# Performance work log

Measured on AMD Instinct MI355X. Metric: run time of the kernel, lower is better.

Reference implementation:

```python
import jax, jax.numpy as jnp
import numpy as np

D_HEAD = 64
MASK_FILL = -1000000.0


def setup_inputs() -> dict:
    key = jax.random.key(0)
    ks = jax.random.split(key, 5)
    batch, seq, d_model, n_heads, d_head = 4, 2048, 1024, 16, D_HEAD
    # xavier_uniform bound for [d_model, n_heads, d_head]: treated as fan_in=d_model, fan_out=n_heads*d_head
    bound_qkv = float(np.sqrt(6.0 / (d_model + n_heads * d_head)))
    bound_out = float(np.sqrt(6.0 / (d_head + n_heads * d_model)))
    return {
        "resid": jax.random.normal(ks[0], (batch, seq, d_model), dtype=jnp.float32),
        "W_Q": jax.random.uniform(ks[1], (d_model, n_heads, d_head), jnp.float32, -bound_qkv, bound_qkv),
        "W_K": jax.random.uniform(ks[2], (d_model, n_heads, d_head), jnp.float32, -bound_qkv, bound_qkv),
        "W_V": jax.random.uniform(ks[3], (d_model, n_heads, d_head), jnp.float32, -bound_qkv, bound_qkv),
        "W_out": jax.random.uniform(ks[4], (d_head, n_heads, d_model), jnp.float32, -bound_out, bound_out),
        "b_out": jnp.zeros((d_model,), dtype=jnp.float32),
    }


def reference(resid, W_Q, W_K, W_V, W_out, b_out):
    # resid: [b, s, d]; W_Q/K/V: [d, h, dh]; W_out: [dh, h, d]
    seq = resid.shape[1]
    d_head = W_Q.shape[-1]
    q = jnp.einsum('bsd,dhk->bshk', resid, W_Q)
    k = jnp.einsum('bsd,dhk->bshk', resid, W_K)
    v = jnp.einsum('bsd,dhk->bshk', resid, W_V)
    scores = jnp.einsum('bqhk,bkhd->bhqd', q, k.astype(q.dtype)) if False else jnp.einsum('bqhc,bshc->bhqs', q, k)
    scores = scores / jnp.sqrt(jnp.asarray(d_head, dtype=scores.dtype))
    causal_mask = jnp.triu(jnp.ones((seq, seq), dtype=bool), k=1)
    scores = jnp.where(causal_mask, MASK_FILL, scores)
    probs = jax.nn.softmax(scores, axis=-1)  # [b, h, q, s]
    z = jnp.einsum('bhqs,bshc->bqhc', probs, v)
    out = jnp.einsum('bqhc,chd->bqd', z, W_out) + b_out
    return out
```

## Files before the change

### kernel.cpp

```cpp
#include <hip/hip_runtime.h>
#include <hip/hip_bf16.h>


typedef short s16x8 __attribute__((ext_vector_type(8)));
typedef short s16x4 __attribute__((ext_vector_type(4)));
typedef float f32x4 __attribute__((ext_vector_type(4)));

#define MFMA_BF16(A, B, C) __builtin_amdgcn_mfma_f32_16x16x32_bf16((A), (B), (C), 0, 0, 0)

#if __has_builtin(__builtin_amdgcn_exp2f)
#define EXP2(x) __builtin_amdgcn_exp2f(x)
#else
#define EXP2(x) exp2f(x)
#endif
#if __has_builtin(__builtin_amdgcn_rcpf)
#define RCP(x) __builtin_amdgcn_rcpf(x)
#else
#define RCP(x) (1.0f / (x))
#endif

__device__ __forceinline__ short f2bf(float f) {
    __bf16 h = (__bf16)f;
    return __builtin_bit_cast(short, h);
}

__device__ __forceinline__ void gld16(const unsigned short* g, unsigned short* l) {
    __builtin_amdgcn_global_load_lds(
        (const __attribute__((address_space(1))) unsigned int*)g,
        (__attribute__((address_space(3))) unsigned int*)l, 16, 0, 0);
}

__global__ __launch_bounds__(256) void prep_fused(
    const float* __restrict__ resid, const float* __restrict__ WQ,
    const float* __restrict__ WK, const float* __restrict__ WV,
    const float* __restrict__ Wout,
    unsigned short* __restrict__ residb, unsigned short* __restrict__ Wqkvt,
    unsigned short* __restrict__ W2t)
{
    const int bid = blockIdx.x;
    if (bid < 8192) {
        const int i = bid * 256 + threadIdx.x;
        const float4 v = ((const float4*)resid)[i];
        s16x4 o;
        o[0] = f2bf(v.x); o[1] = f2bf(v.y); o[2] = f2bf(v.z); o[3] = f2bf(v.w);
        *(s16x4*)(residb + (size_t)i * 4) = o;
        return;
    }
    __shared__ unsigned short tile[64][66];
    const int id2 = bid - 8192;
    const int which = id2 >> 8;
    const int sub = id2 & 255;
    const int tx = threadIdx.x & 63, ty = threadIdx.x >> 6;
    if (which < 3) {
        const float* W = which == 0 ? WQ : (which == 1 ? WK : WV);
        unsigned short* Wt = Wqkvt + (size_t)which * 1024 * 1024;
        const int n0 = (sub & 15) * 64, k0 = (sub >> 4) * 64;
        #pragma unroll
        for (int i = ty; i < 64; i += 4)
            tile[i][tx] = (unsigned short)f2bf(W[(size_t)(k0 + i) * 1024 + n0 + tx]);
        __syncthreads();
        #pragma unroll
        for (int i = ty; i < 64; i += 4)
            Wt[(size_t)(n0 + i) * 1024 + k0 + tx] = tile[tx][i];
    } else {
        const int d0 = (sub & 15) * 64, h = sub >> 4;
        #pragma unroll
        for (int c = ty; c < 64; c += 4)
            tile[c][tx] = (unsigned short)f2bf(Wout[(size_t)(c * 16 + h) * 1024 + d0 + tx]);
        __syncthreads();
        #pragma unroll
        for (int i = ty; i < 64; i += 4)
            W2t[(size_t)(d0 + i) * 1024 + h * 64 + tx] = tile[tx][i];
    }
}

template <int MODE>
__global__ __launch_bounds__(256, 2) void gemm_bt(
    const unsigned short* __restrict__ A,
    const unsigned short* __restrict__ Bt,
    float* __restrict__ Cf, const float* __restrict__ bias,
    unsigned short* __restrict__ Qb, unsigned short* __restrict__ Kb,
    unsigned short* __restrict__ Vt,
    int M, int N, int K)
{
    __shared__ __align__(16) unsigned short AB[2 * 128 * 72];
    const int tid  = threadIdx.x;
    const int lane = tid & 63;
    const int w    = tid >> 6;
    const int wm   = w & 1, wn = w >> 1;
    const int quad = lane >> 4, fl = lane & 15;
    const int m0 = blockIdx.y * 128, n0 = blockIdx.x * 128;

    const unsigned short* gp[9];
    unsigned ldso[9];
    #pragma unroll
    for (int i = 0; i < 9; ++i) {
        const int c = i * 256 + tid;
        const int cm = c % 1152;
        const int r = cm / 9, cl0 = cm % 9;
        const int cl = (cl0 == 8) ? 0 : cl0;
        gp[i] = (c < 1152 ? A + (size_t)(m0 + r) * K : Bt + (size_t)(n0 + r) * K) + cl * 8;
        ldso[i] = (unsigned)c * 8u;
    }

    f32x4 acc[4][4];
    #pragma unroll
    for (int i = 0; i < 4; ++i)
        #pragma unroll
        for (int j = 0; j < 4; ++j)
            acc[i][j] = (f32x4){0.f, 0.f, 0.f, 0.f};

    for (int kt = 0; kt < K; kt += 64) {
        __syncthreads();
        #pragma unroll
        for (int i = 0; i < 9; ++i)
            gld16(gp[i] + kt, AB + ldso[i]);
        __syncthreads();
        #pragma unroll
        for (int ko = 0; ko < 2; ++ko) {
            s16x8 af[4], bf[4];
            #pragma unroll
            for (int mi = 0; mi < 4; ++mi)
                af[mi] = *(const s16x8*)(AB + (wm * 64 + mi * 16 + fl) * 72 + ko * 32 + quad * 8);
            #pragma unroll
            for (int ni = 0; ni < 4; ++ni)
                bf[ni] = *(const s16x8*)(AB + 9216 + (wn * 64 + ni * 16 + fl) * 72 + ko * 32 + quad * 8);
            #pragma unroll
            for (int mi = 0; mi < 4; ++mi)
                #pragma unroll
                for (int ni = 0; ni < 4; ++ni)
                    acc[mi][ni] = MFMA_BF16(af[mi], bf[ni], acc[mi][ni]);
        }
    }

    if (MODE == 0) {
        #pragma unroll
        for (int ni = 0; ni < 4; ++ni) {
            const int col = n0 + wn * 64 + ni * 16 + fl;
            const float bv = bias[col];
            #pragma unroll
            for (int mi = 0; mi < 4; ++mi) {
                const int row = m0 + wm * 64 + mi * 16 + quad * 4;
                #pragma unroll
                for (int r = 0; r < 4; ++r)
                    Cf[(size_t)(row + r) * N + col] = acc[mi][ni][r] + bv;
            }
        }
    } else {
        #pragma unroll
        for (int ni = 0; ni < 4; ++ni) {
            const int colg = n0 + wn * 64 + ni * 16 + fl;
            #pragma unroll
            for (int mi = 0; mi < 4; ++mi) {
                const int token = m0 + wm * 64 + mi * 16 + quad * 4;
                if (n0 < 1024) {
                    #pragma unroll
                    for (int r = 0; r < 4; ++r)
                        Qb[(size_t)(token + r) * 1024 + colg] = (unsigned short)f2bf(acc[mi][ni][r]);
                } else if (n0 < 2048) {
                    #pragma unroll
                    for (int r = 0; r < 4; ++r)
                        Kb[(size_t)(token + r) * 1024 + (colg - 1024)] = (unsigned short)f2bf(acc[mi][ni][r]);
                } else {
                    const int cc = colg - 2048;
                    const int hh = cc >> 6, cl = cc & 63;
                    const int bb = token >> 11, ss = token & 2047;
                    s16x4 pv;
                    pv[0] = f2bf(acc[mi][ni][0]); pv[1] = f2bf(acc[mi][ni][1]);
                    pv[2] = f2bf(acc[mi][ni][2]); pv[3] = f2bf(acc[mi][ni][3]);
                    *(s16x4*)(Vt + (size_t)((bb * 16 + hh) * 64 + cl) * 2048 + ss) = pv;
                }
            }
        }
    }
}

template <bool DIAG>
__device__ __forceinline__ void attn_tile(
    int s0, int wl, int wq0, int fl, int quad,
    const unsigned short* __restrict__ KV, const unsigned short* __restrict__ Vs,
    unsigned short* __restrict__ PbW,
    const s16x8 (&qfr)[2][2], f32x4 (&zt)[2][4], float (&ls)[2])
{
    const float SC = 0.18033688011112042f;
    const float M  = 32.0f;
    #pragma unroll
    for (int c4 = 0; c4 < 4; ++c4) {
        if (DIAG && c4 > wl) break;
        #pragma unroll
        for (int e = 0; e < 2; ++e) {
            const int f = 2 * c4 + e;
            const unsigned short* Krow = KV + (f * 16 + fl) * 72;
            const s16x8 kf0 = *(const s16x8*)(Krow + quad * 8);
            const s16x8 kf1 = *(const s16x8*)(Krow + 32 + quad * 8);
            #pragma unroll
            for (int g = 0; g < 2; ++g) {
                unsigned short* pw = PbW + (g * 16 + fl) * 36 + e * 16 + quad * 4;
                if (DIAG && f > 2 * wl + g) {
                    *(s16x4*)pw = (s16x4){0, 0, 0, 0};
                } else {
                    f32x4 z = (f32x4){0.f, 0.f, 0.f, 0.f};
                    z = MFMA_BF16(kf0, qfr[g][0], z);
                    z = MFMA_BF16(kf1, qfr[g][1], z);
                    float p[4];
                    #pragma unroll
                    for (int r = 0; r < 4; ++r) {
                        float arg = fmaf(z[r], SC, -M);
                        if (DIAG && f == 2 * wl + g) {
                            const int s = s0 + f * 16 + quad * 4 + r;
                            const int qi = wq0 + g * 16 + fl;
                            if (s > qi) arg = -100.f;
                        }
                        p[r] = EXP2(arg);
                    }
                    ls[g] += (p[0] + p[1]) + (p[2] + p[3]);
                    s16x4 pk;
                    pk[0] = f2bf(p[0]); pk[1] = f2bf(p[1]);
                    pk[2] = f2bf(p[2]); pk[3] = f2bf(p[3]);
                    *(s16x4*)pw = pk;
                }
            }
        }
        const s16x8 pf0 = *(const s16x8*)(PbW + fl * 36 + quad * 8);
        const s16x8 pf1 = *(const s16x8*)(PbW + (16 + fl) * 36 + quad * 8);
        #pragma unroll
        for (int mf = 0; mf < 4; ++mf) {
            const s16x8 vf = *(const s16x8*)(Vs + (mf * 16 + fl) * 136 + c4 * 32 + quad * 8);
            zt[0][mf] = MFMA_BF16(vf, pf0, zt[0][mf]);
            zt[1][mf] = MFMA_BF16(vf, pf1, zt[1][mf]);
        }
    }
}

__global__ __launch_bounds__(512, 4) void attn_causal(
    const unsigned short* __restrict__ Qb,
    const unsigned short* __restrict__ Kb,
    const unsigned short* __restrict__ Vt,
    unsigned short* __restrict__ Zb)
{
    __shared__ __align__(16) unsigned short KV[17920];
    __shared__ __align__(16) unsigned short Pb[8][32 * 36];
    const int tid = threadIdx.x, lane = tid & 63, w = tid >> 6;
    const int quad = lane >> 4, fl = lane & 15;
    const int lid = blockIdx.x;
    const int g8 = lid >> 6;
    const int qb = g8 < 4 ? 7 - g8 : g8 - 4;
    const int bh = lid & 63, b = bh >> 4, h = bh & 15;
    const int wq0 = qb * 256 + w * 32;
    const int wl = w & 3;
    const int dt = 2 * qb + (w >> 2);

    const unsigned short* Kbase = Kb + (size_t)b * 2048 * 1024 + h * 64;
    const unsigned short* Vbase = Vt + (size_t)bh * 64 * 2048;
    unsigned short* PbW = Pb[w];
    const unsigned short* Vs = KV + 9216;

    s16x8 qfr[2][2];
    #pragma unroll
    for (int g = 0; g < 2; ++g) {
        const unsigned short* Qrow = Qb + (size_t)(b * 2048 + wq0 + g * 16 + fl) * 1024 + h * 64;
        qfr[g][0] = *(const s16x8*)(Qrow + quad * 8);
        qfr[g][1] = *(const s16x8*)(Qrow + 32 + quad * 8);
    }

    const unsigned short* gsp[5];
    int sadv[5];
    unsigned ldsb[5];
    #pragma unroll
    for (int i = 0; i < 5; ++i) {
        const int W = w + 8 * i;
        if (W < 35) {
            const int c = W * 64 + lane;
            if (c < 1152) {
                const int r = c / 9, cl0 = c % 9;
                const int cl = (cl0 == 8) ? 0 : cl0;
                gsp[i] = Kbase + r * 1024 + cl * 8;  sadv[i] = 128 * 1024;
            } else {
                const int cc = c - 1152;
                const int r = cc / 17, cl0 = cc % 17;
                const int cl = (cl0 == 16) ? 0 : cl0;
                gsp[i] = Vbase + r * 2048 + cl * 8;  sadv[i] = 128;
            }
            ldsb[i] = (unsigned)c * 8u;
        }
    }

    f32x4 zt[2][4];
    #pragma unroll
    for (int g = 0; g < 2; ++g)
        #pragma unroll
        for (int mf = 0; mf < 4; ++mf) zt[g][mf] = (f32x4){0.f, 0.f, 0.f, 0.f};
    float ls[2] = {0.f, 0.f};
    const int ntiles = 2 * qb + 2;

    for (int kt = 0; kt < ntiles; ++kt) {
        __syncthreads();
        #pragma unroll
        for (int i = 0; i < 5; ++i)
            if (w + 8 * i < 35)
                gld16(gsp[i], KV + ldsb[i]);
        #pragma unroll
        for (int i = 0; i < 5; ++i)
            if (w + 8 * i < 35)
                gsp[i] += sadv[i];
        __syncthreads();

        if (kt < dt) {
            attn_tile<false>(kt << 7, wl, wq0, fl, quad, KV, Vs, PbW, qfr, zt, ls);
        } else if (kt == dt) {
            attn_tile<true>(kt << 7, wl, wq0, fl, quad, KV, Vs, PbW, qfr, zt, ls);
        }
    }
    #pragma unroll
    for (int g = 0; g < 2; ++g) {
        float lt = ls[g];
        lt += __shfl_xor(lt, 16);
        lt += __shfl_xor(lt, 32);
        const float inv = RCP(lt);
        unsigned short* Zrow = Zb + (size_t)(b * 2048 + wq0 + g * 16 + fl) * 1024 + h * 64;
        #pragma unroll
        for (int mf = 0; mf < 4; ++mf) {
            s16x4 o;
            o[0] = f2bf(zt[g][mf][0] * inv); o[1] = f2bf(zt[g][mf][1] * inv);
            o[2] = f2bf(zt[g][mf][2] * inv); o[3] = f2bf(zt[g][mf][3] * inv);
            *(s16x4*)(Zrow + mf * 16 + quad * 4) = o;
        }
    }
}

extern "C" void kernel_launch(void* const* d_in, const int* in_sizes, int n_in,
                              void* d_out, int out_size, void* d_ws, size_t ws_size,
                              hipStream_t stream) {
    const float* resid = (const float*)d_in[0];
    const float* WQ    = (const float*)d_in[1];
    const float* WK    = (const float*)d_in[2];
    const float* WV    = (const float*)d_in[3];
    const float* Wout  = (const float*)d_in[4];
    const float* bout  = (const float*)d_in[5];
    float* out = (float*)d_out;

    char* p = (char*)d_ws;
    auto alloc = [&](size_t bytes) { void* r = (void*)p; p += (bytes + 255) & ~(size_t)255; return r; };
    unsigned short* residb = (unsigned short*)alloc(8192ull * 1024 * 2);
    unsigned short* Wqkvt  = (unsigned short*)alloc(3072ull * 1024 * 2);
    unsigned short* W2t    = (unsigned short*)alloc(1024ull * 1024 * 2);
    unsigned short* Qbuf   = (unsigned short*)alloc(8192ull * 1024 * 2);
    unsigned short* Kbuf   = (unsigned short*)alloc(8192ull * 1024 * 2);
    unsigned short* Vtb    = (unsigned short*)alloc(64ull * 64 * 2048 * 2);
    unsigned short* Zbuf   = (unsigned short*)alloc(8192ull * 1024 * 2);

    prep_fused<<<9216, 256, 0, stream>>>(resid, WQ, WK, WV, Wout, residb, Wqkvt, W2t);
    gemm_bt<1><<<dim3(24, 64), 256, 0, stream>>>(residb, Wqkvt, nullptr, nullptr,
                                                 Qbuf, Kbuf, Vtb, 8192, 3072, 1024);
    attn_causal<<<512, 512, 0, stream>>>(Qbuf, Kbuf, Vtb, Zbuf);
    gemm_bt<0><<<dim3(8, 64), 256, 0, stream>>>(Zbuf, W2t, out, bout,
                                                nullptr, nullptr, nullptr, 8192, 1024, 1024);
}
```

Measured before the change: 255.4 us.

## Give each attention wave 64 query rows with 256-thread blocks

The attention kernel now runs 4 waves per block instead of 8, and each wave handles 64 query rows (4 groups of 16) instead of 32. Each K and V fragment read from LDS is reused across four MFMA groups, which cuts LDS traffic per FLOP. The P staging buffer is double-buffered per c4 step. The cost is many more accumulator registers per thread, lower occupancy (launch bounds 256,2), coarser causal-diagonal work balance within a wave, and more global-to-LDS load instructions per thread for each tile.

```diff
diff --git a/kernel.cpp b/kernel.cpp
--- a/kernel.cpp
+++ b/kernel.cpp
@@ -177,16 +177,17 @@
 
 template <bool DIAG>
 __device__ __forceinline__ void attn_tile(
-    int s0, int wl, int wq0, int fl, int quad,
+    int s0, int mw, int wq0, int fl, int quad,
     const unsigned short* __restrict__ KV, const unsigned short* __restrict__ Vs,
     unsigned short* __restrict__ PbW,
-    const s16x8 (&qfr)[2][2], f32x4 (&zt)[2][4], float (&ls)[2])
+    const s16x8 (&qfr)[4][2], f32x4 (&zt)[4][4], float (&ls)[4])
 {
     const float SC = 0.18033688011112042f;
     const float M  = 32.0f;
     #pragma unroll
     for (int c4 = 0; c4 < 4; ++c4) {
-        if (DIAG && c4 > wl) break;
+        if (DIAG && c4 > ((mw + 3) >> 1)) break;
+        unsigned short* pb = PbW + (c4 & 1) * (64 * 36);
         #pragma unroll
         for (int e = 0; e < 2; ++e) {
             const int f = 2 * c4 + e;
@@ -194,9 +195,9 @@
             const s16x8 kf0 = *(const s16x8*)(Krow + quad * 8);
             const s16x8 kf1 = *(const s16x8*)(Krow + 32 + quad * 8);
             #pragma unroll
-            for (int g = 0; g < 2; ++g) {
-                unsigned short* pw = PbW + (g * 16 + fl) * 36 + e * 16 + quad * 4;
-                if (DIAG && f > 2 * wl + g) {
+            for (int g = 0; g < 4; ++g) {
+                unsigned short* pw = pb + (g * 16 + fl) * 36 + e * 16 + quad * 4;
+                if (DIAG && f > mw + g) {
                     *(s16x4*)pw = (s16x4){0, 0, 0, 0};
                 } else {
                     f32x4 z = (f32x4){0.f, 0.f, 0.f, 0.f};
@@ -206,7 +207,7 @@
                     #pragma unroll
                     for (int r = 0; r < 4; ++r) {
                         float arg = fmaf(z[r], SC, -M);
-                        if (DIAG && f == 2 * wl + g) {
+                        if (DIAG && f == mw + g) {
                             const int s = s0 + f * 16 + quad * 4 + r;
                             const int qi = wq0 + g * 16 + fl;
                             if (s > qi) arg = -100.f;
@@ -221,54 +222,57 @@
                 }
             }
         }
-        const s16x8 pf0 = *(const s16x8*)(PbW + fl * 36 + quad * 8);
-        const s16x8 pf1 = *(const s16x8*)(PbW + (16 + fl) * 36 + quad * 8);
+        s16x8 pf[4];
+        #pragma unroll
+        for (int g = 0; g < 4; ++g)
+            pf[g] = *(const s16x8*)(pb + (g * 16 + fl) * 36 + quad * 8);
         #pragma unroll
         for (int mf = 0; mf < 4; ++mf) {
             const s16x8 vf = *(const s16x8*)(Vs + (mf * 16 + fl) * 136 + c4 * 32 + quad * 8);
-            zt[0][mf] = MFMA_BF16(vf, pf0, zt[0][mf]);
-            zt[1][mf] = MFMA_BF16(vf, pf1, zt[1][mf]);
-        }
-    }
-}
-
-__global__ __launch_bounds__(512, 4) void attn_causal(
+            #pragma unroll
+            for (int g = 0; g < 4; ++g)
+                zt[g][mf] = MFMA_BF16(vf, pf[g], zt[g][mf]);
+        }
+    }
+}
+
+__global__ __launch_bounds__(256, 2) void attn_causal(
     const unsigned short* __restrict__ Qb,
     const unsigned short* __restrict__ Kb,
     const unsigned short* __restrict__ Vt,
     unsigned short* __restrict__ Zb)
 {
     __shared__ __align__(16) unsigned short KV[17920];
-    __shared__ __align__(16) unsigned short Pb[8][32 * 36];
+    __shared__ __align__(16) unsigned short Pb[4][2][64 * 36];
     const int tid = threadIdx.x, lane = tid & 63, w = tid >> 6;
     const int quad = lane >> 4, fl = lane & 15;
     const int lid = blockIdx.x;
     const int g8 = lid >> 6;
     const int qb = g8 < 4 ? 7 - g8 : g8 - 4;
     const int bh = lid & 63, b = bh >> 4, h = bh & 15;
-    const int wq0 = qb * 256 + w * 32;
-    const int wl = w & 3;
-    const int dt = 2 * qb + (w >> 2);
+    const int wq0 = qb * 256 + w * 64;
+    const int mw = (w & 1) * 4;
+    const int dt = 2 * qb + (w >> 1);
 
     const unsigned short* Kbase = Kb + (size_t)b * 2048 * 1024 + h * 64;
     const unsigned short* Vbase = Vt + (size_t)bh * 64 * 2048;
-    unsigned short* PbW = Pb[w];
+    unsigned short* PbW = Pb[w][0];
     const unsigned short* Vs = KV + 9216;
 
-    s16x8 qfr[2][2];
-    #pragma unroll
-    for (int g = 0; g < 2; ++g) {
+    s16x8 qfr[4][2];
+    #pragma unroll
+    for (int g = 0; g < 4; ++g) {
         const unsigned short* Qrow = Qb + (size_t)(b * 2048 + wq0 + g * 16 + fl) * 1024 + h * 64;
         qfr[g][0] = *(const s16x8*)(Qrow + quad * 8);
         qfr[g][1] = *(const s16x8*)(Qrow + 32 + quad * 8);
     }
 
-    const unsigned short* gsp[5];
-    int sadv[5];
-    unsigned ldsb[5];
-    #pragma unroll
-    for (int i = 0; i < 5; ++i) {
-        const int W = w + 8 * i;
+    const unsigned short* gsp[9];
+    int sadv[9];
+    unsigned ldsb[9];
+    #pragma unroll
+    for (int i = 0; i < 9; ++i) {
+        const int W = w + 4 * i;
         if (W < 35) {
             const int c = W * 64 + lane;
             if (c < 1152) {
@@ -285,34 +289,34 @@
         }
     }
 
-    f32x4 zt[2][4];
-    #pragma unroll
-    for (int g = 0; g < 2; ++g)
+    f32x4 zt[4][4];
+    #pragma unroll
+    for (int g = 0; g < 4; ++g)
         #pragma unroll
         for (int mf = 0; mf < 4; ++mf) zt[g][mf] = (f32x4){0.f, 0.f, 0.f, 0.f};
-    float ls[2] = {0.f, 0.f};
+    float ls[4] = {0.f, 0.f, 0.f, 0.f};
     const int ntiles = 2 * qb + 2;
 
     for (int kt = 0; kt < ntiles; ++kt) {
         __syncthreads();
         #pragma unroll
-        for (int i = 0; i < 5; ++i)
-            if (w + 8 * i < 35)
+        for (int i = 0; i < 9; ++i)
+            if (w + 4 * i < 35)
                 gld16(gsp[i], KV + ldsb[i]);
         #pragma unroll
-        for (int i = 0; i < 5; ++i)
-            if (w + 8 * i < 35)
+        for (int i = 0; i < 9; ++i)
+            if (w + 4 * i < 35)
                 gsp[i] += sadv[i];
         __syncthreads();
 
         if (kt < dt) {
-            attn_tile<false>(kt << 7, wl, wq0, fl, quad, KV, Vs, PbW, qfr, zt, ls);
+            attn_tile<false>(kt << 7, mw, wq0, fl, quad, KV, Vs, PbW, qfr, zt, ls);
         } else if (kt == dt) {
-            attn_tile<true>(kt << 7, wl, wq0, fl, quad, KV, Vs, PbW, qfr, zt, ls);
-        }
-    }
-    #pragma unroll
-    for (int g = 0; g < 2; ++g) {
+            attn_tile<true>(kt << 7, mw, wq0, fl, quad, KV, Vs, PbW, qfr, zt, ls);
+        }
+    }
+    #pragma unroll
+    for (int g = 0; g < 4; ++g) {
         float lt = ls[g];
         lt += __shfl_xor(lt, 16);
         lt += __shfl_xor(lt, 32);
@@ -352,7 +356,7 @@
     prep_fused<<<9216, 256, 0, stream>>>(resid, WQ, WK, WV, Wout, residb, Wqkvt, W2t);
     gemm_bt<1><<<dim3(24, 64), 256, 0, stream>>>(residb, Wqkvt, nullptr, nullptr,
                                                  Qbuf, Kbuf, Vtb, 8192, 3072, 1024);
-    attn_causal<<<512, 512, 0, stream>>>(Qbuf, Kbuf, Vtb, Zbuf);
+    attn_causal<<<512, 256, 0, stream>>>(Qbuf, Kbuf, Vtb, Zbuf);
     gemm_bt<0><<<dim3(8, 64), 256, 0, stream>>>(Zbuf, W2t, out, bout,
                                                 nullptr, nullptr, nullptr, 8192, 1024, 1024);
 }
```

Result: slower. 268.2 us (+5.0%).
